# Performance work log

Measured on AMD Instinct MI355X. Metric: run time of the kernel, lower is better.

Reference implementation:

```python
import jax, jax.numpy as jnp
import numpy as np

HEADS = 4

def gat_layer(x, W, a_src, a_dst, bias, edge_index, n):
    # PyG-style GATConv with self-loops, heads averaged (concat=False) so out dim == hidden_dim
    H, C = a_src.shape
    h = (x @ W).reshape(n, H, C)                      # [N,H,C]
    loops = jnp.arange(n)
    src = jnp.concatenate([edge_index[0], loops])
    dst = jnp.concatenate([edge_index[1], loops])
    e = jax.nn.leaky_relu((h * a_src).sum(-1)[src] + (h * a_dst).sum(-1)[dst], 0.2)  # [E,H]
    m = jax.ops.segment_max(e, dst, num_segments=n)   # segment softmax over incoming edges
    ex = jnp.exp(e - m[dst])
    s = jax.ops.segment_sum(ex, dst, num_segments=n)
    alpha = ex / (s[dst] + 1e-16)
    out = jax.ops.segment_sum(alpha[:, :, None] * h[src], dst, num_segments=n)  # [N,H,C]
    return out.mean(axis=1) + bias

def setup_inputs() -> dict:
    key = jax.random.key(0)
    ks = jax.random.split(key, 24)
    Nd, Ni, Ne = 20000, 4096, 4096
    D_in, D = 512, 256
    n_int, n_emo = 64, 32
    inp = {}
    inp['dialogue_embeddings'] = jax.random.normal(ks[0], (Nd, D_in), jnp.float32)
    inp['intention_indices'] = jax.random.randint(ks[1], (Ni,), 0, n_int)
    inp['emotion_indices'] = jax.random.randint(ks[2], (Ne,), 0, n_emo)
    inp['dialogue_edge_index'] = jax.random.randint(ks[3], (2, Nd * 32), 0, Nd)
    inp['intention_edge_index'] = jax.random.randint(ks[4], (2, Ni * 16), 0, Ni)
    inp['emotion_edge_index'] = jax.random.randint(ks[5], (2, Ne * 16), 0, Ne)
    s = lambda k, shape: jax.random.normal(k, shape, jnp.float32) * 0.02
    inp['intention_emb'] = s(ks[6], (n_int, D))
    inp['emotion_emb'] = s(ks[7], (n_emo, D))
    inp['Wd'] = s(ks[8], (D_in, HEADS * D)); inp['a_src_d'] = s(ks[9], (HEADS, D)); inp['a_dst_d'] = s(ks[10], (HEADS, D)); inp['bd'] = jnp.zeros((D,), jnp.float32)
    inp['Wi'] = s(ks[11], (D, HEADS * D)); inp['a_src_i'] = s(ks[12], (HEADS, D)); inp['a_dst_i'] = s(ks[13], (HEADS, D)); inp['bi'] = jnp.zeros((D,), jnp.float32)
    inp['We'] = s(ks[14], (D, HEADS * D)); inp['a_src_e'] = s(ks[15], (HEADS, D)); inp['a_dst_e'] = s(ks[16], (HEADS, D)); inp['be'] = jnp.zeros((D,), jnp.float32)
    inp['W_dfc'] = s(ks[17], (D, D)); inp['b_dfc'] = jnp.zeros((D,), jnp.float32)
    inp['W_ifc'] = s(ks[18], (D, D)); inp['b_ifc'] = jnp.zeros((D,), jnp.float32)
    inp['W_efc'] = s(ks[19], (D, D)); inp['b_efc'] = jnp.zeros((D,), jnp.float32)
    inp['W_fc'] = s(ks[20], (3 * D, n_emo)); inp['b_fc'] = jnp.zeros((n_emo,), jnp.float32)
    return inp

def reference(dialogue_embeddings, intention_indices, emotion_indices,
              dialogue_edge_index, intention_edge_index, emotion_edge_index,
              intention_emb, emotion_emb,
              Wd, a_src_d, a_dst_d, bd, Wi, a_src_i, a_dst_i, bi,
              We, a_src_e, a_dst_e, be,
              W_dfc, b_dfc, W_ifc, b_ifc, W_efc, b_efc, W_fc, b_fc):
    Nd = dialogue_embeddings.shape[0]
    Ni = intention_indices.shape[0]
    Ne = emotion_indices.shape[0]
    ie = intention_emb[intention_indices]   # [Ni, D]
    ee = emotion_emb[emotion_indices]       # [Ne, D]
    d = gat_layer(dialogue_embeddings, Wd, a_src_d, a_dst_d, bd, dialogue_edge_index, Nd)
    d = jax.nn.relu(d @ W_dfc + b_dfc)
    i = gat_layer(ie, Wi, a_src_i, a_dst_i, bi, intention_edge_index, Ni)
    i = jax.nn.relu(i @ W_ifc + b_ifc)
    e = gat_layer(ee, We, a_src_e, a_dst_e, be, emotion_edge_index, Ne)
    e = jax.nn.relu(e @ W_efc + b_efc)
    iw = jax.nn.softmax(d @ i.T, axis=-1)   # [Nd, Ni]
    att_i = iw @ i                           # [Nd, D]
    ew = jax.nn.softmax(d @ e.T, axis=-1)   # [Nd, Ne]
    att_e = ew @ e                           # [Nd, D]
    inputs = jnp.concatenate([d, att_i, att_e], axis=-1)  # [Nd, 3D]
    return inputs @ W_fc + b_fc
```

## Files before the change

kernel.cpp:

```cpp
#include <hip/hip_runtime.h>
#include <hip/hip_bf16.h>
#include <math.h>

#define DEV static __device__ __forceinline__

typedef __attribute__((ext_vector_type(8))) short short8;
typedef __attribute__((ext_vector_type(4))) short short4v;
typedef __attribute__((ext_vector_type(4))) float f32x4;
typedef __attribute__((ext_vector_type(2))) long long2v;

DEV float bf2f(__hip_bfloat16 x) { return __bfloat162float(x); }
DEV __hip_bfloat16 f2bf(float x) { return __float2bfloat16(x); }
DEV short bfbits(float x) { __hip_bfloat16 h = __float2bfloat16(x); short s; __builtin_memcpy(&s, &h, 2); return s; }
DEV float b2f_bits(short s) { __hip_bfloat16 h; __builtin_memcpy(&h, &s, 2); return __bfloat162float(h); }
DEV float lrelu(float x) { return x > 0.f ? x : 0.2f * x; }

DEV float load_in(const void* p, long long i, bool f32) {
  return f32 ? ((const float*)p)[i] : bf2f(((const __hip_bfloat16*)p)[i]);
}

DEV long pack8_fp8(const float* f) {
  int lo = 0, hi = 0;
  lo = __builtin_amdgcn_cvt_pk_fp8_f32(f[0], f[1], lo, false);
  lo = __builtin_amdgcn_cvt_pk_fp8_f32(f[2], f[3], lo, true);
  hi = __builtin_amdgcn_cvt_pk_fp8_f32(f[4], f[5], hi, false);
  hi = __builtin_amdgcn_cvt_pk_fp8_f32(f[6], f[7], hi, true);
  return ((long)(unsigned)hi << 32) | (unsigned)lo;
}

DEV f32x4 mfma_fp8(long a, long b, f32x4 c) {
  return __builtin_amdgcn_mfma_f32_16x16x32_fp8_fp8(a, b, c, 0, 0, 0);
}

__global__ void HGAN_45148696215914_kernel() {}

__global__ void fill_k(__hip_bfloat16* __restrict__ p, float v, int n)
{
  int i = blockIdx.x * blockDim.x + threadIdx.x;
  if (i < n) p[i] = __float2bfloat16(v);
}

struct DetectArgs { const unsigned int* p[23]; int nw[23]; int id[23]; };

__global__ void detect_k(DetectArgs a, int* __restrict__ flags)
{
  __shared__ int cnt_sh;
  if (threadIdx.x == 0) cnt_sh = 0;
  __syncthreads();
  const unsigned int* w = a.p[blockIdx.x];
  int nwords = a.nw[blockIdx.x];
  int bad = 0;
  for (int i = threadIdx.x; i < nwords; i += blockDim.x) {
    unsigned int x = w[i];
    float v0 = __uint_as_float((x & 0xffffu) << 16);
    float v1 = __uint_as_float(x & 0xffff0000u);
    if (!(fabsf(v0) <= 1e4f)) bad++;
    if (!(fabsf(v1) <= 1e4f)) bad++;
  }
  atomicAdd(&cnt_sh, bad);
  __syncthreads();
  if (threadIdx.x == 0) flags[a.id[blockIdx.x]] = (cnt_sh > nwords / 4) ? 1 : 0;
}

struct CvArgs {
  const void* in[7]; const int* flag[7]; __hip_bfloat16* out[7];
  int K[7], N[7], NL[7], toff[7]; int nseg;
};

__global__ __launch_bounds__(256) void convtrN_k(CvArgs a)
{
  __shared__ __hip_bfloat16 t[32][33];
  int b = blockIdx.x;
  int s = 0;
  while (s + 1 < a.nseg && b >= a.toff[s + 1]) ++s;
  int ti = b - a.toff[s];
  int kb = a.K[s] >> 5;
  int bk = ti % kb, bn = ti / kb;
  const void* in = a.in[s];
  const int* flag = a.flag[s];
  __hip_bfloat16* out = a.out[s];
  int K = a.K[s], N = a.N[s];
  const bool f = flag && *flag;
  int lx = threadIdx.x & 31, ly = threadIdx.x >> 5;
  int gn = bn * 32 + lx;
#pragma unroll
  for (int rr = 0; rr < 32; rr += 8)
    t[rr + ly][lx] = (gn < N)
        ? f2bf(load_in(in, (long long)(bk * 32 + rr + ly) * N + gn, f))
        : f2bf(0.f);
  __syncthreads();
#pragma unroll
  for (int rr = 0; rr < 32; rr += 8)
    out[(size_t)(bn * 32 + rr + ly) * K + bk * 32 + lx] = t[lx][rr + ly];
}

DEV void mgemm_body(
    const void* A, const int* aflag, int lda, const int* idxA,
    const __hip_bfloat16* BT, void* C, int ldc,
    const void* bias, const int* biasflag, int relu,
    int permC, int M, int K, int Nlim, const int* cflag,
    int m0, int n0, __hip_bfloat16* Ash, __hip_bfloat16* Bsh)
{
  const bool af = aflag && *aflag;
  const bool bsf = biasflag && *biasflag;
  const bool cf = cflag && *cflag;
  const int tid = threadIdx.x;
  const int wv = tid >> 6, lane = tid & 63, qd = lane >> 4, lm = lane & 15;
  const int wr = wv >> 1, wc = wv & 1;

  f32x4 acc[4][4];
#pragma unroll
  for (int i = 0; i < 4; ++i)
    for (int j = 0; j < 4; ++j)
      for (int v = 0; v < 4; ++v) acc[i][j][v] = 0.f;

  for (int k0 = 0; k0 < K; k0 += 64) {
    __syncthreads();
    for (int u = tid; u < 1024; u += 256) {
      int r = u >> 3, cu = u & 7;
      int gm = m0 + r;
      short8 vv;
      if (gm < M) {
        long long row = idxA ? idxA[gm] : gm;
        long long basei = row * (long long)lda + k0 + cu * 8;
        if (af) {
          const float4* fp = (const float4*)((const float*)A + basei);
          float4 f0 = fp[0], f1 = fp[1];
          vv[0] = bfbits(f0.x); vv[1] = bfbits(f0.y);
          vv[2] = bfbits(f0.z); vv[3] = bfbits(f0.w);
          vv[4] = bfbits(f1.x); vv[5] = bfbits(f1.y);
          vv[6] = bfbits(f1.z); vv[7] = bfbits(f1.w);
        } else {
          vv = *(const short8*)((const __hip_bfloat16*)A + basei);
        }
      } else {
#pragma unroll
        for (int j = 0; j < 8; ++j) vv[j] = 0;
      }
      *(short8*)(&Ash[r * 72 + cu * 8]) = vv;
    }
    for (int u = tid; u < 1024; u += 256) {
      int r = u >> 3, cu = u & 7;
      *(short8*)(&Bsh[r * 72 + cu * 8]) =
          *(const short8*)(BT + (size_t)(n0 + r) * K + k0 + cu * 8);
    }
    __syncthreads();
#pragma unroll
    for (int ks = 0; ks < 2; ++ks) {
      short8 a[4], b[4];
#pragma unroll
      for (int i = 0; i < 4; ++i)
        a[i] = *(const short8*)(&Ash[(wr * 64 + i * 16 + lm) * 72 + ks * 32 + qd * 8]);
#pragma unroll
      for (int j = 0; j < 4; ++j)
        b[j] = *(const short8*)(&Bsh[(wc * 64 + j * 16 + lm) * 72 + ks * 32 + qd * 8]);
#pragma unroll
      for (int i = 0; i < 4; ++i)
#pragma unroll
        for (int j = 0; j < 4; ++j)
          acc[i][j] = __builtin_amdgcn_mfma_f32_16x16x32_bf16(a[i], b[j], acc[i][j], 0, 0, 0);
    }
  }
#pragma unroll
  for (int j = 0; j < 4; ++j) {
    int gn = n0 + wc * 64 + j * 16 + lm;
    if (gn >= Nlim) continue;
    float bv = bias ? load_in(bias, gn, bsf) : 0.f;
    int gcol = permC ? ((gn & 255) * 4 + (gn >> 8)) : gn;
#pragma unroll
    for (int i = 0; i < 4; ++i) {
#pragma unroll
      for (int v = 0; v < 4; ++v) {
        int gm = m0 + wr * 64 + i * 16 + qd * 4 + v;
        if (gm >= M) continue;
        float x = acc[i][j][v] + bv;
        if (relu) x = fmaxf(x, 0.f);
        long long idx = (long long)gm * ldc + gcol;
        if (cf) ((float*)C)[idx] = x;
        else    ((__hip_bfloat16*)C)[idx] = f2bf(x);
      }
    }
  }
}

__global__ __launch_bounds__(256) void mgemm_k(
    const void* __restrict__ A, const int* __restrict__ aflag, int lda,
    const int* __restrict__ idxA,
    const __hip_bfloat16* __restrict__ BT,
    void* __restrict__ C, int ldc,
    const void* __restrict__ bias, const int* __restrict__ biasflag, int relu,
    int permC, int M, int N, int K, int Nlim,
    const int* __restrict__ cflag)
{
  __shared__ __align__(16) __hip_bfloat16 Ash[128 * 72];
  __shared__ __align__(16) __hip_bfloat16 Bsh[128 * 72];
  (void)N;
  mgemm_body(A, aflag, lda, idxA, BT, C, ldc, bias, biasflag, relu,
             permC, M, K, Nlim, cflag,
             blockIdx.y * 128, blockIdx.x * 128, Ash, Bsh);
}

struct SegArgs {
  const void* A[3]; const int* aflag[3]; int lda[3]; const int* idxA[3];
  const __hip_bfloat16* BT[3]; void* C[3]; int ldc[3];
  const void* bias[3]; const int* bflag[3];
  int M[3]; int K[3]; int yoff[3];
  int relu, permC, Nlim;
};

__global__ __launch_bounds__(256) void mgemm_seg_k(SegArgs a)
{
  __shared__ __align__(16) __hip_bfloat16 Ash[128 * 72];
  __shared__ __align__(16) __hip_bfloat16 Bsh[128 * 72];
  int y = blockIdx.y;
  int s = (y >= a.yoff[2]) ? 2 : ((y >= a.yoff[1]) ? 1 : 0);
  mgemm_body(a.A[s], a.aflag[s], a.lda[s], a.idxA[s], a.BT[s], a.C[s], a.ldc[s],
             a.bias[s], a.bflag[s], a.relu, a.permC, a.M[s], a.K[s], a.Nlim,
             nullptr, (y - a.yoff[s]) * 128, blockIdx.x * 128, Ash, Bsh);
}

__global__ __launch_bounds__(256) void score3_k(
    const __hip_bfloat16* __restrict__ hI,
    const void* as1, const void* ad1, const int* sf1, const int* df1,
    const void* as2, const void* ad2, const int* sf2, const int* df2,
    const void* as3, const void* ad3, const int* sf3, const int* df3,
    int s1, int s2,
    float* __restrict__ ss, float* __restrict__ ds,
    int* __restrict__ cnt, int N)
{
  __shared__ float red[4][8];
  int n = blockIdx.x, c = threadIdx.x;
  if (c == 0) cnt[n] = 0;
  const void* a_src; const void* a_dst; const int* sfp; const int* dfp;
  if (n < s1)      { a_src = as1; a_dst = ad1; sfp = sf1; dfp = df1; }
  else if (n < s2) { a_src = as2; a_dst = ad2; sfp = sf2; dfp = df2; }
  else             { a_src = as3; a_dst = ad3; sfp = sf3; dfp = df3; }
  const bool sf = sfp && *sfp;
  const bool df = dfp && *dfp;
  short4v hv = *(const short4v*)(hI + (size_t)n * 1024 + c * 4);
  float h0 = b2f_bits(hv[0]), h1 = b2f_bits(hv[1]);
  float h2 = b2f_bits(hv[2]), h3 = b2f_bits(hv[3]);
  float r0 = h0 * load_in(a_src, 0 * 256 + c, sf);
  float r1 = h1 * load_in(a_src, 1 * 256 + c, sf);
  float r2 = h2 * load_in(a_src, 2 * 256 + c, sf);
  float r3 = h3 * load_in(a_src, 3 * 256 + c, sf);
  float t0 = h0 * load_in(a_dst, 0 * 256 + c, df);
  float t1 = h1 * load_in(a_dst, 1 * 256 + c, df);
  float t2 = h2 * load_in(a_dst, 2 * 256 + c, df);
  float t3 = h3 * load_in(a_dst, 3 * 256 + c, df);
#pragma unroll
  for (int o = 32; o > 0; o >>= 1) {
    r0 += __shfl_down(r0, o); r1 += __shfl_down(r1, o);
    r2 += __shfl_down(r2, o); r3 += __shfl_down(r3, o);
    t0 += __shfl_down(t0, o); t1 += __shfl_down(t1, o);
    t2 += __shfl_down(t2, o); t3 += __shfl_down(t3, o);
  }
  int wv = c >> 6, lane = c & 63;
  if (lane == 0) {
    red[wv][0] = r0; red[wv][1] = r1; red[wv][2] = r2; red[wv][3] = r3;
    red[wv][4] = t0; red[wv][5] = t1; red[wv][6] = t2; red[wv][7] = t3;
  }
  __syncthreads();
  if (c < 8) {
    float s = red[0][c] + red[1][c] + red[2][c] + red[3][c];
    if (c < 4) ss[n * 4 + c] = s;
    else       ds[n * 4 + (c - 4)] = s;
  }
}

__global__ void count3_k(const int* __restrict__ d1, int E1,
                         const int* __restrict__ d2, int E2, int o2,
                         const int* __restrict__ d3, int E3, int o3,
                         int* __restrict__ cnt)
{
  int k = blockIdx.x * blockDim.x + threadIdx.x;
  if (k < E1) atomicAdd(&cnt[d1[k]], 1);
  else if (k < E1 + E2) atomicAdd(&cnt[d2[k - E1] + o2], 1);
  else if (k < E1 + E2 + E3) atomicAdd(&cnt[d3[k - E1 - E2] + o3], 1);
}

__global__ __launch_bounds__(1024) void scan1_k(
    const int* __restrict__ cnt, int* __restrict__ offp, int* __restrict__ bsum, int n)
{
  __shared__ int sh[1024];
  int idx = blockIdx.x * 1024 + (int)threadIdx.x;
  int v = (idx < n) ? cnt[idx] : 0;
  sh[threadIdx.x] = v;
  __syncthreads();
  for (int d = 1; d < 1024; d <<= 1) {
    int t = (threadIdx.x >= (unsigned)d) ? sh[threadIdx.x - d] : 0;
    __syncthreads();
    sh[threadIdx.x] += t;
    __syncthreads();
  }
  if (idx < n) offp[idx] = sh[threadIdx.x] - v;
  if (threadIdx.x == 1023) bsum[blockIdx.x] = sh[1023];
}

__global__ void scan3_k(int* __restrict__ offp, const int* __restrict__ bsum,
                        int* __restrict__ cur, int n, int nb)
{
  int i = blockIdx.x * blockDim.x + threadIdx.x;
  if (i < n) {
    int chunk = i >> 10;
    int pre = 0;
    for (int b = 0; b < chunk; ++b) pre += bsum[b];
    int v = offp[i] + pre;
    offp[i] = v;
    cur[i] = v;
    if (i == n - 1) {
      int tot = 0;
      for (int b = 0; b < nb; ++b) tot += bsum[b];
      offp[n] = tot;
    }
  }
}

__global__ void scatter3_k(const int* __restrict__ s1, const int* __restrict__ d1, int E1,
                           const int* __restrict__ s2, const int* __restrict__ d2, int E2, int o2,
                           const int* __restrict__ s3, const int* __restrict__ d3, int E3, int o3,
                           int* __restrict__ cur, int* __restrict__ srcs)
{
  int k = blockIdx.x * blockDim.x + threadIdx.x;
  if (k < E1) {
    int p = atomicAdd(&cur[d1[k]], 1);
    srcs[p] = s1[k];
  } else if (k < E1 + E2) {
    int kk = k - E1;
    int p = atomicAdd(&cur[d2[kk] + o2], 1);
    srcs[p] = s2[kk] + o2;
  } else if (k < E1 + E2 + E3) {
    int kk = k - E1 - E2;
    int p = atomicAdd(&cur[d3[kk] + o3], 1);
    srcs[p] = s3[kk] + o3;
  }
}

__global__ __launch_bounds__(256) void agg3_k(
    const __hip_bfloat16* __restrict__ hI,
    const float* __restrict__ ss, const float* __restrict__ ds,
    const int* __restrict__ offp, const int* __restrict__ srcs,
    const void* b1, const int* bf1,
    const void* b2, const int* bf2,
    const void* b3, const int* bf3,
    int s1, int s2,
    __hip_bfloat16* __restrict__ outp, int N)
{
  __shared__ int src_sh[64];
  __shared__ __align__(16) float w_sh[64][4];
  __shared__ float scale_sh[4];
  __shared__ float l_sh[4];
  __shared__ __align__(16) float pair_sh[128][8];
  int n = blockIdx.x;
  int c = threadIdx.x;
  int hd_w = c >> 6;
  int e_w  = c & 63;
  int half = c >> 7;
  int tc   = c & 127;
  int s0 = offp[n], deg = offp[n + 1] - s0;
  int total = deg + 1;
  float dsn = ds[n * 4 + hd_w];
  float m_run = -1e30f, l_run = 0.f;
  float A0[4] = {0.f, 0.f, 0.f, 0.f};
  float A1[4] = {0.f, 0.f, 0.f, 0.f};
  for (int base = 0; base < total; base += 64) {
    int cnt = min(64, total - base);
    __syncthreads();
    if (c < cnt) src_sh[c] = (base + c == 0) ? n : srcs[s0 + base + c - 1];
    __syncthreads();
    float val = -1e30f;
    if (e_w < cnt) val = lrelu(ss[src_sh[e_w] * 4 + hd_w] + dsn);
    float vmax = val;
#pragma unroll
    for (int o = 32; o > 0; o >>= 1) vmax = fmaxf(vmax, __shfl_xor(vmax, o));
    float newm = fmaxf(m_run, vmax);
    float p = (e_w < cnt) ? __expf(val - newm) : 0.f;
    float psum = p;
#pragma unroll
    for (int o = 32; o > 0; o >>= 1) psum += __shfl_xor(psum, o);
    float sc = __expf(m_run - newm);
    l_run = l_run * sc + psum;
    m_run = newm;
    w_sh[e_w][hd_w] = p;
    if (e_w == 0) scale_sh[hd_w] = sc;
    __syncthreads();
    float sc0 = scale_sh[0], sc1 = scale_sh[1], sc2 = scale_sh[2], sc3 = scale_sh[3];
    A0[0] *= sc0; A0[1] *= sc1; A0[2] *= sc2; A0[3] *= sc3;
    A1[0] *= sc0; A1[1] *= sc1; A1[2] *= sc2; A1[3] *= sc3;
    for (int e = half; e < cnt; e += 2) {
      short8 hv = *(const short8*)(hI + (size_t)src_sh[e] * 1024 + tc * 8);
      float4 w = *(const float4*)(&w_sh[e][0]);
      A0[0] += w.x * b2f_bits(hv[0]); A0[1] += w.y * b2f_bits(hv[1]);
      A0[2] += w.z * b2f_bits(hv[2]); A0[3] += w.w * b2f_bits(hv[3]);
      A1[0] += w.x * b2f_bits(hv[4]); A1[1] += w.y * b2f_bits(hv[5]);
      A1[2] += w.z * b2f_bits(hv[6]); A1[3] += w.w * b2f_bits(hv[7]);
    }
  }
  __syncthreads();
  if (e_w == 0) l_sh[hd_w] = l_run;
  if (half == 1) {
    *(float4*)(&pair_sh[tc][0]) = make_float4(A0[0], A0[1], A0[2], A0[3]);
    *(float4*)(&pair_sh[tc][4]) = make_float4(A1[0], A1[1], A1[2], A1[3]);
  }
  __syncthreads();
  if (half == 0) {
    float4 p0 = *(const float4*)(&pair_sh[tc][0]);
    float4 p1 = *(const float4*)(&pair_sh[tc][4]);
    A0[0] += p0.x; A0[1] += p0.y; A0[2] += p0.z; A0[3] += p0.w;
    A1[0] += p1.x; A1[1] += p1.y; A1[2] += p1.z; A1[3] += p1.w;
    const void* bias; const int* bfp;
    if (n < s1)      { bias = b1; bfp = bf1; }
    else if (n < s2) { bias = b2; bfp = bf2; }
    else             { bias = b3; bfp = bf3; }
    const bool bf = bfp && *bfp;
    float il0 = 1.f / (l_sh[0] + 1e-16f), il1 = 1.f / (l_sh[1] + 1e-16f);
    float il2 = 1.f / (l_sh[2] + 1e-16f), il3 = 1.f / (l_sh[3] + 1e-16f);
    float r0 = 0.25f * (A0[0] * il0 + A0[1] * il1 + A0[2] * il2 + A0[3] * il3);
    float r1 = 0.25f * (A1[0] * il0 + A1[1] * il1 + A1[2] * il2 + A1[3] * il3);
    outp[(size_t)n * 256 + 2 * tc]     = f2bf(r0 + load_in(bias, 2 * tc, bf));
    outp[(size_t)n * 256 + 2 * tc + 1] = f2bf(r1 + load_in(bias, 2 * tc + 1, bf));
  }
}

__global__ __launch_bounds__(256) void conv8_k(
    const __hip_bfloat16* __restrict__ in0, char* __restrict__ K8_0, char* __restrict__ KT8_0,
    const __hip_bfloat16* __restrict__ in1, char* __restrict__ K8_1, char* __restrict__ KT8_1,
    int Nk)
{
  __shared__ __align__(16) __hip_bfloat16 t[32][264];
  const __hip_bfloat16* in = blockIdx.y ? in1 : in0;
  char* K8  = blockIdx.y ? K8_1  : K8_0;
  char* KT8 = blockIdx.y ? KT8_1 : KT8_0;
  int kv0 = blockIdx.x * 32;
  size_t tbase = (size_t)(kv0 >> 5) * 8192;
  int tid = threadIdx.x;
  (void)Nk;
  for (int u = tid; u < 1024; u += 256) {
    int r = u >> 5, c = u & 31;
    *(short8*)(&t[r][c * 8]) = *(const short8*)(in + (size_t)(kv0 + r) * 256 + c * 8);
  }
  __syncthreads();
  for (int u = tid; u < 1024; u += 256) {
    int r = u >> 5, g = u & 31, pos = g * 8;
    int qd_ = pos >> 6, s = (pos >> 3) & 7;
    int d = s * 32 + qd_ * 8;
    float f[8];
#pragma unroll
    for (int j = 0; j < 8; ++j) f[j] = 16.f * bf2f(t[r][d + j]);
    int c16 = pos >> 4, h = (pos >> 3) & 1;
    int unit = ((c16 & 3) * 2 + (r >> 4)) * 64 + (c16 >> 2) * 16 + (r & 15);
    *(long*)(K8 + tbase + (size_t)unit * 16 + h * 8) = pack8_fp8(f);
  }
  {
    int d = tid;
#pragma unroll
    for (int g = 0; g < 4; ++g) {
      float f[8];
#pragma unroll
      for (int j = 0; j < 8; ++j) f[j] = 16.f * bf2f(t[g * 8 + j][d]);
      int unit = (d >> 4) * 64 + g * 16 + (d & 15);
      *(long*)(KT8 + tbase + (size_t)unit * 8) = pack8_fp8(f);
    }
  }
}

__global__ __launch_bounds__(256, 4) void flashf8_k(
    const __hip_bfloat16* __restrict__ Q, int ldq,
    const char* __restrict__ K8_0, const char* __restrict__ KT8_0,
    const char* __restrict__ K8_1, const char* __restrict__ KT8_1,
    __hip_bfloat16* __restrict__ Out, int ldo,
    int M, int Nk)
{
  __shared__ __align__(16) char Ksh8[2][8192];
  __shared__ __align__(16) char KTsh8[2][8192];
  __shared__ __align__(16) char Psh8[4][16 * 40];
  const int att = blockIdx.y;
  const char* K8  = att ? K8_1  : K8_0;
  const char* KT8 = att ? KT8_1 : KT8_0;
  __hip_bfloat16* Outp = Out + att * 256;

  const int tid = threadIdx.x;
  const int wv = tid >> 6, lane = tid & 63;
  const int qd = lane >> 4, lm = lane & 15;
  const int r0 = blockIdx.x * 64 + wv * 16;
  char* Pw = Psh8[wv];

  long qf8[8];
  {
    const bool ok = (r0 + lm) < M;
    const __hip_bfloat16* qrow = Q + (size_t)(r0 + lm) * ldq;
#pragma unroll
    for (int s = 0; s < 8; ++s) {
      float f[8];
      if (ok) {
        short8 qv = *(const short8*)(qrow + s * 32 + qd * 8);
#pragma unroll
        for (int j = 0; j < 8; ++j) f[j] = 16.f * b2f_bits(qv[j]);
      } else {
#pragma unroll
        for (int j = 0; j < 8; ++j) f[j] = 0.f;
      }
      qf8[s] = pack8_fp8(f);
    }
  }

  f32x4 Oacc[16];
#pragma unroll
  for (int i = 0; i < 16; ++i)
    for (int v = 0; v < 4; ++v) Oacc[i][v] = 0.f;
  float mrow = -1e30f, lrow = 0.f;

  {
    short8 k0 = *(const short8*)(K8 + (size_t)tid * 16);
    short8 k1 = *(const short8*)(K8 + (size_t)(tid + 256) * 16);
    short8 t0 = *(const short8*)(KT8 + (size_t)tid * 16);
    short8 t1 = *(const short8*)(KT8 + (size_t)(tid + 256) * 16);
    *(short8*)(&Ksh8[0][tid * 16]) = k0;
    *(short8*)(&Ksh8[0][(tid + 256) * 16]) = k1;
    *(short8*)(&KTsh8[0][tid * 16]) = t0;
    *(short8*)(&KTsh8[0][(tid + 256) * 16]) = t1;
  }
  __syncthreads();

  int iter = 0;
  for (int n0 = 0; n0 < Nk; n0 += 32, ++iter) {
    const int cur = iter & 1, nxt = cur ^ 1;
    const bool havenext = (n0 + 32) < Nk;
    short8 pk0, pk1, pt0, pt1;
    if (havenext) {
      size_t tb = (size_t)(iter + 1) * 8192;
      pk0 = *(const short8*)(K8 + tb + (size_t)tid * 16);
      pk1 = *(const short8*)(K8 + tb + (size_t)(tid + 256) * 16);
      pt0 = *(const short8*)(KT8 + tb + (size_t)tid * 16);
      pt1 = *(const short8*)(KT8 + tb + (size_t)(tid + 256) * 16);
    }
    const char* Kc  = Ksh8[cur];
    const char* KTc = KTsh8[cur];

    f32x4 S[2];
#pragma unroll
    for (int t = 0; t < 2; ++t)
      for (int v = 0; v < 4; ++v) S[t][v] = 0.f;
#pragma unroll
    for (int sp = 0; sp < 4; ++sp) {
#pragma unroll
      for (int t = 0; t < 2; ++t) {
        long2v a2 = *(const long2v*)(&Kc[((sp * 2 + t) * 64 + lane) * 16]);
        S[t] = mfma_fp8(a2[0], qf8[2 * sp],     S[t]);
        S[t] = mfma_fp8(a2[1], qf8[2 * sp + 1], S[t]);
      }
    }
#pragma unroll
    for (int t = 0; t < 2; ++t)
      for (int v = 0; v < 4; ++v) S[t][v] *= 0.00390625f;

    float tmax = -1e30f;
#pragma unroll
    for (int t = 0; t < 2; ++t)
      for (int v = 0; v < 4; ++v) tmax = fmaxf(tmax, S[t][v]);
    tmax = fmaxf(tmax, __shfl_xor(tmax, 16));
    tmax = fmaxf(tmax, __shfl_xor(tmax, 32));
    float newm = fmaxf(mrow, tmax);
    float psum = 0.f;
#pragma unroll
    for (int t = 0; t < 2; ++t)
      for (int v = 0; v < 4; ++v) {
        float p = __expf(S[t][v] - newm);
        S[t][v] = p;
        psum += p;
      }
    psum += __shfl_xor(psum, 16);
    psum += __shfl_xor(psum, 32);
    float scale = __expf(mrow - newm);
    lrow = lrow * scale + psum;
    mrow = newm;
#pragma unroll
    for (int t = 0; t < 2; ++t) {
      int pk = __builtin_amdgcn_cvt_pk_fp8_f32(16.f * S[t][0], 16.f * S[t][1], 0, false);
      pk = __builtin_amdgcn_cvt_pk_fp8_f32(16.f * S[t][2], 16.f * S[t][3], pk, true);
      *(int*)(&Pw[lm * 40 + t * 16 + qd * 4]) = pk;
    }

    if (__any(scale < 1.0f)) {
      float scl[4];
#pragma unroll
      for (int v = 0; v < 4; ++v) scl[v] = __shfl(scale, qd * 4 + v);
#pragma unroll
      for (int i = 0; i < 16; ++i)
        for (int v = 0; v < 4; ++v) Oacc[i][v] *= scl[v];
    }

    {
      long pa0 = *(const long*)(&Pw[lm * 40 + qd * 8]);
#pragma unroll
      for (int dt = 0; dt < 16; ++dt) {
        long b = *(const long*)(&KTc[dt * 512 + lane * 8]);
        Oacc[dt] = mfma_fp8(pa0, b, Oacc[dt]);
      }
    }

    if (havenext) {
      *(short8*)(&Ksh8[nxt][tid * 16]) = pk0;
      *(short8*)(&Ksh8[nxt][(tid + 256) * 16]) = pk1;
      *(short8*)(&KTsh8[nxt][tid * 16]) = pt0;
      *(short8*)(&KTsh8[nxt][(tid + 256) * 16]) = pt1;
    }
    __syncthreads();
  }

  {
    float linv = 1.f / (256.f * lrow);
    float li[4];
#pragma unroll
    for (int v = 0; v < 4; ++v) li[v] = __shfl(linv, qd * 4 + v);
#pragma unroll
    for (int v = 0; v < 4; ++v) {
      int grow = r0 + qd * 4 + v;
      if (grow >= M) continue;
#pragma unroll
      for (int dt = 0; dt < 16; ++dt)
        Outp[(size_t)grow * ldo + dt * 16 + lm] = f2bf(Oacc[dt][v] * li[v]);
    }
  }
}

extern "C" void kernel_launch(void* const* d_in, const int* in_sizes, int n_in,
                              void* d_out, int out_size, void* d_ws, size_t ws_size,
                              hipStream_t stream)
{
  const void* Xd      = d_in[0];
  const int*  int_idx = (const int*)d_in[1];
  const int*  emo_idx = (const int*)d_in[2];
  const int*  ed_d    = (const int*)d_in[3];
  const int*  ed_i    = (const int*)d_in[4];
  const int*  ed_e    = (const int*)d_in[5];
  const void* int_emb = d_in[6];
  const void* emo_emb = d_in[7];
  const void* Wd = d_in[8],  *a_src_d = d_in[9],  *a_dst_d = d_in[10], *bd = d_in[11];
  const void* Wi = d_in[12], *a_src_i = d_in[13], *a_dst_i = d_in[14], *bi = d_in[15];
  const void* We = d_in[16], *a_src_e = d_in[17], *a_dst_e = d_in[18], *be = d_in[19];
  const void* W_dfc = d_in[20], *b_dfc = d_in[21];
  const void* W_ifc = d_in[22], *b_ifc = d_in[23];
  const void* W_efc = d_in[24], *b_efc = d_in[25];
  const void* W_fc  = d_in[26], *b_fc  = d_in[27];

  const int DIn  = in_sizes[8] / 1024;
  const int Nd   = in_sizes[0] / DIn;
  const int Ni   = in_sizes[1];
  const int Ne   = in_sizes[2];
  const int Ed   = in_sizes[3] / 2;
  const int Ei   = in_sizes[4] / 2;
  const int Ee   = in_sizes[5] / 2;
  const int Nout = in_sizes[27];
  const int NU   = Nd + Ni + Ne;

  char* base = (char*)d_ws;
  size_t off = 0;
  auto alloc = [&](size_t nbytes) -> void* {
    void* p = base + off;
    off = (off + nbytes + 255) & ~(size_t)255;
    return p;
  };
  int* flags = (int*)alloc(32 * sizeof(int));
  int* bsum  = (int*)alloc(64 * sizeof(int));
  __hip_bfloat16* hbuf = (__hip_bfloat16*)alloc((size_t)NU * 1024 * 2);
  __hip_bfloat16* cat  = (__hip_bfloat16*)alloc((size_t)Nd * 768 * 2);
  __hip_bfloat16* gat_tmp = (__hip_bfloat16*)alloc((size_t)NU * 256 * 2);
  __hip_bfloat16* WdT  = (__hip_bfloat16*)alloc((size_t)1024 * DIn * 2);
  __hip_bfloat16* WiT  = (__hip_bfloat16*)alloc((size_t)1024 * 256 * 2);
  __hip_bfloat16* WeT  = (__hip_bfloat16*)alloc((size_t)1024 * 256 * 2);
  __hip_bfloat16* WdfT = (__hip_bfloat16*)alloc((size_t)256 * 256 * 2);
  __hip_bfloat16* WifT = (__hip_bfloat16*)alloc((size_t)256 * 256 * 2);
  __hip_bfloat16* WefT = (__hip_bfloat16*)alloc((size_t)256 * 256 * 2);
  __hip_bfloat16* WfcT = (__hip_bfloat16*)alloc((size_t)128 * 768 * 2);
  float* ss  = (float*)alloc((size_t)NU * 4 * 4);
  float* dsb = (float*)alloc((size_t)NU * 4 * 4);
  int* cnt   = (int*)alloc((size_t)NU * 4);
  int* offp  = (int*)alloc((size_t)(NU + 1) * 4);
  int* cur   = (int*)alloc((size_t)NU * 4);
  int* srcs  = (int*)alloc((size_t)(Ed + Ei + Ee) * 4);
  const size_t need = off;
  (void)n_in;

  __hip_bfloat16* i_mat = hbuf;
  __hip_bfloat16* e_mat = hbuf + (size_t)Ni * 256;
  char* K8i  = (char*)(hbuf + (size_t)2 * Ni * 256);
  char* KT8i = K8i + (size_t)Ni * 256;
  char* K8e  = KT8i + (size_t)Ni * 256;
  char* KT8e = K8e + (size_t)Ne * 256;

  const dim3 T(256);
  if (ws_size < need) {
    fill_k<<<(out_size + 255) / 256, T, 0, stream>>>((__hip_bfloat16*)d_out, 0.25f, out_size);
    return;
  }

  {
    DetectArgs da;
    const int fid[23] = {0,6,7,8,9,10,11,12,13,14,15,16,17,18,19,20,21,22,23,24,25,26,27};
    for (int t = 0; t < 23; ++t) {
      int id = fid[t];
      int nw = in_sizes[id] / 2;
      if (nw > 2048) nw = 2048;
      if (nw < 1) nw = 1;
      da.p[t] = (const unsigned int*)d_in[id];
      da.nw[t] = nw;
      da.id[t] = id;
    }
    detect_k<<<23, 256, 0, stream>>>(da, flags);
  }
  #define F(i) (flags + (i))

  {
    CvArgs cv;
    const void* ins[7]  = {Wd, Wi, We, W_dfc, W_ifc, W_efc, W_fc};
    const int*  fgs[7]  = {F(8), F(12), F(16), F(20), F(22), F(24), F(26)};
    __hip_bfloat16* outs[7] = {WdT, WiT, WeT, WdfT, WifT, WefT, WfcT};
    int Ks[7]  = {DIn, 256, 256, 256, 256, 256, 768};
    int Ns[7]  = {1024, 1024, 1024, 256, 256, 256, Nout};
    int NLs[7] = {1024, 1024, 1024, 256, 256, 256, 128};
    int run = 0;
    for (int s = 0; s < 7; ++s) {
      cv.in[s] = ins[s]; cv.flag[s] = fgs[s]; cv.out[s] = outs[s];
      cv.K[s] = Ks[s]; cv.N[s] = Ns[s]; cv.NL[s] = NLs[s]; cv.toff[s] = run;
      run += (Ks[s] / 32) * (NLs[s] / 32);
    }
    cv.nseg = 7;
    convtrN_k<<<run, T, 0, stream>>>(cv);
  }

  const int yNd = (Nd + 127) / 128, yNi = Ni / 128, yNe = Ne / 128;
  {
    SegArgs sa;
    sa.A[0] = Xd;      sa.aflag[0] = F(0); sa.lda[0] = DIn; sa.idxA[0] = nullptr;
    sa.BT[0] = WdT;    sa.C[0] = hbuf;     sa.ldc[0] = 1024;
    sa.bias[0] = nullptr; sa.bflag[0] = nullptr; sa.M[0] = Nd; sa.K[0] = DIn;
    sa.A[1] = int_emb; sa.aflag[1] = F(6); sa.lda[1] = 256; sa.idxA[1] = int_idx;
    sa.BT[1] = WiT;    sa.C[1] = hbuf + (size_t)Nd * 1024; sa.ldc[1] = 1024;
    sa.bias[1] = nullptr; sa.bflag[1] = nullptr; sa.M[1] = Ni; sa.K[1] = 256;
    sa.A[2] = emo_emb; sa.aflag[2] = F(7); sa.lda[2] = 256; sa.idxA[2] = emo_idx;
    sa.BT[2] = WeT;    sa.C[2] = hbuf + (size_t)(Nd + Ni) * 1024; sa.ldc[2] = 1024;
    sa.bias[2] = nullptr; sa.bflag[2] = nullptr; sa.M[2] = Ne; sa.K[2] = 256;
    sa.yoff[0] = 0; sa.yoff[1] = yNd; sa.yoff[2] = yNd + yNi;
    sa.relu = 0; sa.permC = 1; sa.Nlim = 1024;
    mgemm_seg_k<<<dim3(8, yNd + yNi + yNe), T, 0, stream>>>(sa);
  }

  {
    int nb = (NU + 1023) / 1024;
    int Etot = Ed + Ei + Ee;
    score3_k<<<NU, T, 0, stream>>>(hbuf,
        a_src_d, a_dst_d, F(9), F(10),
        a_src_i, a_dst_i, F(13), F(14),
        a_src_e, a_dst_e, F(17), F(18),
        Nd, Nd + Ni, ss, dsb, cnt, NU);
    count3_k<<<(Etot + 255) / 256, T, 0, stream>>>(
        ed_d + Ed, Ed, ed_i + Ei, Ei, Nd, ed_e + Ee, Ee, Nd + Ni, cnt);
    scan1_k<<<nb, 1024, 0, stream>>>(cnt, offp, bsum, NU);
    scan3_k<<<(NU + 255) / 256, T, 0, stream>>>(offp, bsum, cur, NU, nb);
    scatter3_k<<<(Etot + 255) / 256, T, 0, stream>>>(
        ed_d, ed_d + Ed, Ed, ed_i, ed_i + Ei, Ei, Nd,
        ed_e, ed_e + Ee, Ee, Nd + Ni, cur, srcs);
    agg3_k<<<NU, T, 0, stream>>>(hbuf, ss, dsb, offp, srcs,
        bd, F(11), bi, F(15), be, F(19), Nd, Nd + Ni, gat_tmp, NU);
  }

  {
    SegArgs sa;
    sa.A[0] = gat_tmp; sa.aflag[0] = nullptr; sa.lda[0] = 256; sa.idxA[0] = nullptr;
    sa.BT[0] = WdfT;   sa.C[0] = cat;   sa.ldc[0] = 768;
    sa.bias[0] = b_dfc; sa.bflag[0] = F(21); sa.M[0] = Nd; sa.K[0] = 256;
    sa.A[1] = gat_tmp + (size_t)Nd * 256; sa.aflag[1] = nullptr; sa.lda[1] = 256; sa.idxA[1] = nullptr;
    sa.BT[1] = WifT;   sa.C[1] = i_mat; sa.ldc[1] = 256;
    sa.bias[1] = b_ifc; sa.bflag[1] = F(23); sa.M[1] = Ni; sa.K[1] = 256;
    sa.A[2] = gat_tmp + (size_t)(Nd + Ni) * 256; sa.aflag[2] = nullptr; sa.lda[2] = 256; sa.idxA[2] = nullptr;
    sa.BT[2] = WefT;   sa.C[2] = e_mat; sa.ldc[2] = 256;
    sa.bias[2] = b_efc; sa.bflag[2] = F(25); sa.M[2] = Ne; sa.K[2] = 256;
    sa.yoff[0] = 0; sa.yoff[1] = yNd; sa.yoff[2] = yNd + yNi;
    sa.relu = 1; sa.permC = 0; sa.Nlim = 256;
    mgemm_seg_k<<<dim3(2, yNd + yNi + yNe), T, 0, stream>>>(sa);
  }

  conv8_k<<<dim3(Ni / 32, 2), T, 0, stream>>>(i_mat, K8i, KT8i, e_mat, K8e, KT8e, Ni);

  flashf8_k<<<dim3((Nd + 63) / 64, 2), T, 0, stream>>>(
      cat, 768, K8i, KT8i, K8e, KT8e, cat + 256, 768, Nd, Ni);

  mgemm_k<<<dim3(1, (Nd + 127) / 128), T, 0, stream>>>(
      cat, nullptr, 768, nullptr, WfcT, d_out, Nout,
      b_fc, F(27), 0, 0, Nd, 128, 768, Nout, F(0));
}
```

Measured before the change: 865.6 us.

## Split flash attention over key halves and merge partials in separate kernel

The fp8 flash-attention kernel gains a third grid dimension that splits the key sequence into two halves. Each block writes a normalized partial output and its per-row max and sum to scratch. A new merge kernel combines the two halves with log-sum-exp weights into the concatenated buffer. The aim is to double the block count so an undersubscribed GPU is better filled, at the cost of extra partial-output traffic, a bf16 rounding of the partials, and one more launch.

```diff
diff --git a/kernel.cpp b/kernel.cpp
--- a/kernel.cpp
+++ b/kernel.cpp
@@ -468,16 +468,16 @@
     const __hip_bfloat16* __restrict__ Q, int ldq,
     const char* __restrict__ K8_0, const char* __restrict__ KT8_0,
     const char* __restrict__ K8_1, const char* __restrict__ KT8_1,
-    __hip_bfloat16* __restrict__ Out, int ldo,
+    __hip_bfloat16* __restrict__ Opart, float2* __restrict__ ml,
     int M, int Nk)
 {
   __shared__ __align__(16) char Ksh8[2][8192];
   __shared__ __align__(16) char KTsh8[2][8192];
   __shared__ __align__(16) char Psh8[4][16 * 40];
   const int att = blockIdx.y;
+  const int z = blockIdx.z;
   const char* K8  = att ? K8_1  : K8_0;
   const char* KT8 = att ? KT8_1 : KT8_0;
-  __hip_bfloat16* Outp = Out + att * 256;
 
   const int tid = threadIdx.x;
   const int wv = tid >> 6, lane = tid & 63;
@@ -485,6 +485,9 @@
   const int r0 = blockIdx.x * 64 + wv * 16;
   char* Pw = Psh8[wv];
 
+  const int half_tiles = Nk >> 6;
+  const int t0 = z * half_tiles;
+
   long qf8[8];
   {
     const bool ok = (r0 + lm) < M;
@@ -511,24 +514,24 @@
   float mrow = -1e30f, lrow = 0.f;
 
   {
-    short8 k0 = *(const short8*)(K8 + (size_t)tid * 16);
-    short8 k1 = *(const short8*)(K8 + (size_t)(tid + 256) * 16);
-    short8 t0 = *(const short8*)(KT8 + (size_t)tid * 16);
-    short8 t1 = *(const short8*)(KT8 + (size_t)(tid + 256) * 16);
+    size_t tb = (size_t)t0 * 8192;
+    short8 k0 = *(const short8*)(K8 + tb + (size_t)tid * 16);
+    short8 k1 = *(const short8*)(K8 + tb + (size_t)(tid + 256) * 16);
+    short8 t0v = *(const short8*)(KT8 + tb + (size_t)tid * 16);
+    short8 t1v = *(const short8*)(KT8 + tb + (size_t)(tid + 256) * 16);
     *(short8*)(&Ksh8[0][tid * 16]) = k0;
     *(short8*)(&Ksh8[0][(tid + 256) * 16]) = k1;
-    *(short8*)(&KTsh8[0][tid * 16]) = t0;
-    *(short8*)(&KTsh8[0][(tid + 256) * 16]) = t1;
+    *(short8*)(&KTsh8[0][tid * 16]) = t0v;
+    *(short8*)(&KTsh8[0][(tid + 256) * 16]) = t1v;
   }
   __syncthreads();
 
-  int iter = 0;
-  for (int n0 = 0; n0 < Nk; n0 += 32, ++iter) {
-    const int cur = iter & 1, nxt = cur ^ 1;
-    const bool havenext = (n0 + 32) < Nk;
+  for (int it = 0; it < half_tiles; ++it) {
+    const int cur = it & 1, nxt = cur ^ 1;
+    const bool havenext = (it + 1) < half_tiles;
     short8 pk0, pk1, pt0, pt1;
     if (havenext) {
-      size_t tb = (size_t)(iter + 1) * 8192;
+      size_t tb = (size_t)(t0 + it + 1) * 8192;
       pk0 = *(const short8*)(K8 + tb + (size_t)tid * 16);
       pk1 = *(const short8*)(K8 + tb + (size_t)(tid + 256) * 16);
       pt0 = *(const short8*)(KT8 + tb + (size_t)tid * 16);
@@ -609,6 +612,7 @@
   }
 
   {
+    __hip_bfloat16* Op = Opart + (size_t)(z * 2 + att) * M * 256;
     float linv = 1.f / (256.f * lrow);
     float li[4];
 #pragma unroll
@@ -619,9 +623,27 @@
       if (grow >= M) continue;
 #pragma unroll
       for (int dt = 0; dt < 16; ++dt)
-        Outp[(size_t)grow * ldo + dt * 16 + lm] = f2bf(Oacc[dt][v] * li[v]);
-    }
-  }
+        Op[(size_t)grow * 256 + dt * 16 + lm] = f2bf(Oacc[dt][v] * li[v]);
+    }
+    if (lane < 16 && (r0 + lm) < M)
+      ml[(size_t)(z * 2 + att) * M + r0 + lm] = make_float2(mrow, lrow);
+  }
+}
+
+__global__ __launch_bounds__(256) void merge_k(
+    const __hip_bfloat16* __restrict__ Opart, const float2* __restrict__ ml,
+    __hip_bfloat16* __restrict__ Out, int ldo, int M)
+{
+  int row = blockIdx.x, att = blockIdx.y, c = threadIdx.x;
+  float2 a = ml[(size_t)(0 * 2 + att) * M + row];
+  float2 b = ml[(size_t)(1 * 2 + att) * M + row];
+  float Mx = fmaxf(a.x, b.x);
+  float w0 = a.y * __expf(a.x - Mx);
+  float w1 = b.y * __expf(b.x - Mx);
+  float inv = 1.f / (w0 + w1 + 1e-30f);
+  float o0 = bf2f(Opart[((size_t)(0 * 2 + att) * M + row) * 256 + c]);
+  float o1 = bf2f(Opart[((size_t)(1 * 2 + att) * M + row) * 256 + c]);
+  Out[(size_t)row * ldo + att * 256 + c] = f2bf((w0 * o0 + w1 * o1) * inv);
 }
 
 extern "C" void kernel_launch(void* const* d_in, const int* in_sizes, int n_in,
@@ -688,6 +710,9 @@
   char* KT8i = K8i + (size_t)Ni * 256;
   char* K8e  = KT8i + (size_t)Ni * 256;
   char* KT8e = K8e + (size_t)Ne * 256;
+  char* scratch = KT8e + (size_t)Ne * 256;
+  __hip_bfloat16* Opart = (__hip_bfloat16*)scratch;
+  float2* mlbuf = (float2*)(scratch + (size_t)4 * Nd * 256 * 2);
 
   const dim3 T(256);
   if (ws_size < need) {
@@ -783,8 +808,10 @@
 
   conv8_k<<<dim3(Ni / 32, 2), T, 0, stream>>>(i_mat, K8i, KT8i, e_mat, K8e, KT8e, Ni);
 
-  flashf8_k<<<dim3((Nd + 63) / 64, 2), T, 0, stream>>>(
-      cat, 768, K8i, KT8i, K8e, KT8e, cat + 256, 768, Nd, Ni);
+  flashf8_k<<<dim3((Nd + 63) / 64, 2, 2), T, 0, stream>>>(
+      cat, 768, K8i, KT8i, K8e, KT8e, Opart, mlbuf, Nd, Ni);
+
+  merge_k<<<dim3(Nd, 2), T, 0, stream>>>(Opart, mlbuf, cat + 256, 768, Nd);
 
   mgemm_k<<<dim3(1, (Nd + 127) / 128), T, 0, stream>>>(
       cat, nullptr, 768, nullptr, WfcT, d_out, Nout,
```

After: 878.8 us. Within noise of the previous version (+1.5%).
